# Kernel optimization log

Hardware: AMD Instinct MI355X
Metric: run time of the kernel (lower is better)

The kernel has to match this reference:

```python
import jax, jax.numpy as jnp
import numpy as np

B, N, D, H = 4, 2048, 512, 8
KD = D // H  # per-head key/value dim = 64
NORM = 1.0 / np.sqrt(KD).astype(np.float32)


def setup_inputs() -> dict:
    key = jax.random.key(0)
    kq, km, k1, k2, k3 = jax.random.split(key, 5)
    s = 1.0 / np.sqrt(D)
    return {
        "queries": jax.random.normal(kq, (B, N, D), dtype=jnp.float32),
        "mask": jax.random.randint(km, (B, N, N), 0, 2).astype(jnp.bool_),
        "Wq": jax.random.normal(k1, (D, D), dtype=jnp.float32) * s,
        "Wk": jax.random.normal(k2, (D, D), dtype=jnp.float32) * s,
        "Wc": jax.random.normal(k3, (D, D), dtype=jnp.float32) * s,
    }


def reference(queries, mask, Wq, Wk, Wc):
    # Self-attention path (keys=None, values=None): V uses key_embed (Wk).
    Q = (queries @ Wq.T).reshape(B, N, H, KD)  # [B,N,H,kd]
    K = (queries @ Wk.T).reshape(B, N, H, KD)
    V = K  # original code: V = key_embed(queries) when values is None
    scores = NORM * jnp.einsum("bqhd,bkhd->bhqk", Q, K)  # [B,H,N,N]
    scores = jnp.where(mask[:, None, :, :], -jnp.inf, scores)
    attn = jax.nn.softmax(scores, axis=-1)
    out = jnp.einsum("bhqk,bkhd->bqhd", attn, V).reshape(B, N, H * KD)
    return out @ Wc.T  # [B,N,D]
```

## Files before the change

### kernel.cpp

```cpp
#include <hip/hip_runtime.h>
#include <math.h>

#define B_ 4
#define N_ 2048
#define D_ 512
#define H_ 8
#define KD_ 64
#define NORM2_ 0.18033688011112042f

typedef __attribute__((ext_vector_type(8))) short short8;
typedef __attribute__((ext_vector_type(4))) float f32x4;
#define MFMA16(a, b, c) __builtin_amdgcn_mfma_f32_16x16x32_bf16(a, b, c, 0, 0, 0)
#define EXP2(x) __builtin_amdgcn_exp2f(x)

static __device__ __forceinline__ ushort f2bf(float x) {
  union { float f; uint32_t u; } v; v.f = x;
  const uint32_t r = v.u + 0x7fffu + ((v.u >> 16) & 1u);
  return (ushort)(r >> 16);
}

static __device__ __forceinline__ void async16(ushort* lds, const ushort* g) {
  __builtin_amdgcn_global_load_lds(
      (const __attribute__((address_space(1))) uint32_t*)g,
      (__attribute__((address_space(3))) uint32_t*)lds, 16, 0, 0);
}

__global__ __launch_bounds__(256) void prep(const float* __restrict__ q,
                                            const int* __restrict__ mask,
                                            const float* __restrict__ wq,
                                            const float* __restrict__ wk,
                                            const float* __restrict__ wc,
                                            ushort* __restrict__ Xb,
                                            ushort* __restrict__ Wb,
                                            uint32_t* __restrict__ pk) {
  const int bx = blockIdx.x;
  if (bx < 2048) {
    const int lane = threadIdx.x & 63;
    const int wid = ((bx << 8) + threadIdx.x) >> 6;
    for (int i = wid; i < 65536; i += 8192) {
      const int4 m = ((const int4*)mask)[i * 64 + lane];
      uint32_t nib = (uint32_t)(m.x != 0) | ((uint32_t)(m.y != 0) << 1) |
                     ((uint32_t)(m.z != 0) << 2) | ((uint32_t)(m.w != 0) << 3);
      nib |= __shfl_xor(nib, 1) << 4;
      nib |= __shfl_xor(nib, 2) << 8;
      nib |= __shfl_xor(nib, 4) << 16;
      if ((lane & 7) == 0) pk[i * 8 + (lane >> 3)] = nib;
    }
  } else if (bx < 3072) {
    const int i = ((bx - 2048) << 8) + threadIdx.x;
    for (int j = i; j < 1048576; j += 262144) {
      const float4 v = ((const float4*)q)[j];
      ushort4 o; o.x = f2bf(v.x); o.y = f2bf(v.y); o.z = f2bf(v.z); o.w = f2bf(v.w);
      ((ushort4*)Xb)[j] = o;
    }
  } else {
    const int i = ((bx - 3072) << 8) + threadIdx.x;
    for (int j = i; j < 196608; j += 24576) {
      const int wi = j >> 16, off = j & 65535;
      const float* src = (wi == 0) ? wq : (wi == 1) ? wk : wc;
      const float4 v = ((const float4*)src)[off];
      ushort4 o; o.x = f2bf(v.x); o.y = f2bf(v.y); o.z = f2bf(v.z); o.w = f2bf(v.w);
      ((ushort4*)Wb)[j] = o;
    }
  }
}

template <int F32OUT>
__global__ __launch_bounds__(256) void gemm128(const ushort* __restrict__ X,
                                               const ushort* __restrict__ W0,
                                               const ushort* __restrict__ W1,
                                               void* __restrict__ C0,
                                               void* __restrict__ C1,
                                               float s0, float s1) {
  const ushort* Wp = (blockIdx.z == 0) ? W0 : W1;
  void* Cp = (blockIdx.z == 0) ? C0 : C1;
  const float sc = (blockIdx.z == 0) ? s0 : s1;
  const int t = threadIdx.x;
  const int w = t >> 6, lane = t & 63, quad = lane >> 4, c = lane & 15;
  const int wm = w & 1, wn = w >> 1;
  const int n0 = blockIdx.x * 128, m0 = blockIdx.y * 128;
  __shared__ __align__(16) ushort Xs[128][64];
  __shared__ __align__(16) ushort Ws[128][64];
  f32x4 acc[4][4];
#pragma unroll
  for (int i = 0; i < 4; ++i)
#pragma unroll
    for (int j = 0; j < 4; ++j) acc[i][j] = (f32x4){0.f, 0.f, 0.f, 0.f};

  for (int k0 = 0; k0 < D_; k0 += 64) {
    __syncthreads();
#pragma unroll
    for (int g = 0; g < 4; ++g) {
      const int id = w * 256 + g * 64 + lane;
      const int row = id >> 3, lch = id & 7;
      const int gch = lch ^ (row & 7);
      async16(&Xs[row][lch * 8], X + (size_t)(m0 + row) * D_ + k0 + gch * 8);
      async16(&Ws[row][lch * 8], Wp + (size_t)(n0 + row) * D_ + k0 + gch * 8);
    }
    __syncthreads();
#pragma unroll
    for (int s = 0; s < 2; ++s) {
      short8 af[4], bt[4];
#pragma unroll
      for (int i = 0; i < 4; ++i) {
        const int rA = wn * 64 + i * 16 + c;
        af[i] = *(const short8*)&Ws[rA][(((s * 4 + quad) ^ (rA & 7)) & 7) * 8];
        const int rB = wm * 64 + i * 16 + c;
        bt[i] = *(const short8*)&Xs[rB][(((s * 4 + quad) ^ (rB & 7)) & 7) * 8];
      }
#pragma unroll
      for (int i = 0; i < 4; ++i)
#pragma unroll
        for (int j = 0; j < 4; ++j) acc[i][j] = MFMA16(af[i], bt[j], acc[i][j]);
    }
  }
#pragma unroll
  for (int i = 0; i < 4; ++i)
#pragma unroll
    for (int j = 0; j < 4; ++j) {
      const size_t off =
          (size_t)(m0 + wm * 64 + j * 16 + c) * D_ + n0 + wn * 64 + i * 16 + quad * 4;
      if (F32OUT) {
        float4 v; v.x = acc[i][j][0]; v.y = acc[i][j][1]; v.z = acc[i][j][2]; v.w = acc[i][j][3];
        *(float4*)((float*)Cp + off) = v;
      } else {
        ushort4 v; v.x = f2bf(acc[i][j][0] * sc); v.y = f2bf(acc[i][j][1] * sc);
        v.z = f2bf(acc[i][j][2] * sc); v.w = f2bf(acc[i][j][3] * sc);
        *(ushort4*)((ushort*)Cp + off) = v;
      }
    }
}

__global__ __launch_bounds__(256) void attn_mfma(const ushort* __restrict__ Qb,
                                                 const ushort* __restrict__ Kb,
                                                 const uint32_t* __restrict__ pk,
                                                 ushort* __restrict__ Ab) {
  const int qt = blockIdx.x, h = blockIdx.y, b = blockIdx.z;
  const int q0 = qt * 64;
  const int t = threadIdx.x;
  const int w = t >> 6, lane = t & 63, quad = lane >> 4, c = lane & 15;

  __shared__ __align__(16) ushort Qs[64][64];
  __shared__ __align__(16) ushort Ks[64][64];
  __shared__ __align__(16) uint32_t KtU[64][32];
  __shared__ __align__(16) ushort Pq[4][16][72];

#pragma unroll
  for (int g = 0; g < 2; ++g) {
    const int id = (w << 7) + (g << 6) + lane;
    const int row = id >> 3, lch = id & 7;
    const int gch = lch ^ (row & 7);
    async16(&Qs[row][lch * 8], Qb + (size_t)(b * N_ + q0 + row) * D_ + h * 64 + gch * 8);
  }
  __syncthreads();
  const int rq = (w << 4) + c;
  const short8 bq0 = *(const short8*)&Qs[rq][((quad ^ (rq & 7)) & 7) * 8];
  const short8 bq1 = *(const short8*)&Qs[rq][(((4 + quad) ^ (rq & 7)) & 7) * 8];

  float lacc = 0.f;
  f32x4 o[4];
#pragma unroll
  for (int i = 0; i < 4; ++i) o[i] = (f32x4){0.f, 0.f, 0.f, 0.f};

  const int kp = t >> 3, ch = t & 7;
  const ushort* kb0 = Kb + (size_t)(b * N_ + 2 * kp) * D_ + h * 64 + ch * 8;
  const uint32_t* pkq = pk + ((size_t)(b * N_ + q0 + (w << 4) + c) << 6);

  uint4 c0 = *(const uint4*)kb0;
  uint4 c1 = *(const uint4*)(kb0 + D_);
  uint2 cm = *(const uint2*)pkq;
  uint4 nx0, nx1; uint2 nxm;

  const int NT = N_ / 64;
  for (int kt = 0; kt < NT; ++kt) {
    __syncthreads();
    const int r0 = 2 * kp, r1 = r0 + 1;
    *(uint4*)&Ks[r0][((ch ^ (r0 & 7)) & 7) * 8] = c0;
    *(uint4*)&Ks[r1][((ch ^ (r1 & 7)) & 7) * 8] = c1;
    const uint32_t* a0 = (const uint32_t*)&c0;
    const uint32_t* a1 = (const uint32_t*)&c1;
#pragma unroll
    for (int m = 0; m < 4; ++m) {
      const uint32_t lo = __builtin_amdgcn_perm(a1[m], a0[m], 0x05040100);
      const uint32_t hi = __builtin_amdgcn_perm(a1[m], a0[m], 0x07060302);
      const int j0 = 2 * m, j1 = 2 * m + 1;
      KtU[ch * 8 + j0][(kp & 3) | ((((kp >> 2) ^ j0 ^ ch) & 7) << 2)] = lo;
      KtU[ch * 8 + j1][(kp & 3) | ((((kp >> 2) ^ j1 ^ ch) & 7) << 2)] = hi;
    }
    __syncthreads();

    if (kt + 1 < NT) {
      const ushort* kbn = kb0 + (size_t)(kt + 1) * 64 * D_;
      nx0 = *(const uint4*)kbn;
      nx1 = *(const uint4*)(kbn + D_);
      nxm = *(const uint2*)(pkq + (kt + 1) * 2);
    }

#pragma unroll
    for (int tI = 0; tI < 4; ++tI) {
      const int rk = tI * 16 + c;
      const short8 aK0 = *(const short8*)&Ks[rk][((quad ^ (rk & 7)) & 7) * 8];
      const short8 aK1 = *(const short8*)&Ks[rk][(((4 + quad) ^ (rk & 7)) & 7) * 8];
      f32x4 z = (f32x4){0.f, 0.f, 0.f, 0.f};
      z = MFMA16(aK0, bq0, z);
      z = MFMA16(aK1, bq1, z);
      const uint32_t mw = (tI < 2) ? cm.x : cm.y;
      const int bb = ((tI & 1) << 4) + quad * 4;
      float p[4];
#pragma unroll
      for (int r = 0; r < 4; ++r) {
        const float sv = ((mw >> (bb + r)) & 1u) ? -INFINITY : z[r];
        p[r] = EXP2(sv);
        lacc += p[r];
      }
      const uint32_t pw0 =
          __builtin_amdgcn_perm(__float_as_uint(p[1]), __float_as_uint(p[0]), 0x07060302);
      const uint32_t pw1 =
          __builtin_amdgcn_perm(__float_as_uint(p[3]), __float_as_uint(p[2]), 0x07060302);
      *(uint2*)&Pq[w][c][tI * 16 + quad * 4] = make_uint2(pw0, pw1);
    }

    const short8 bp0 = *(const short8*)&Pq[w][c][quad * 8];
    const short8 bp1 = *(const short8*)&Pq[w][c][32 + quad * 8];
#pragma unroll
    for (int dt = 0; dt < 4; ++dt) {
      const int dd = dt * 16 + c;
      const int g = (c & 7) ^ ((2 * dt + (c >> 3)) & 7);
      const short8 aV0 = *(const short8*)&KtU[dd][((quad ^ g) & 7) << 2];
      const short8 aV1 = *(const short8*)&KtU[dd][(((4 + quad) ^ g) & 7) << 2];
      o[dt] = MFMA16(aV0, bp0, o[dt]);
      o[dt] = MFMA16(aV1, bp1, o[dt]);
    }

    if (kt + 1 < NT) { c0 = nx0; c1 = nx1; cm = nxm; }
  }

  float l = lacc;
  l += __shfl_xor(l, 16);
  l += __shfl_xor(l, 32);
  const float inv = 1.f / l;
#pragma unroll
  for (int dt = 0; dt < 4; ++dt) {
    ushort4 v; v.x = f2bf(o[dt][0] * inv); v.y = f2bf(o[dt][1] * inv);
    v.z = f2bf(o[dt][2] * inv); v.w = f2bf(o[dt][3] * inv);
    *(ushort4*)(Ab + (size_t)(b * N_ + q0 + (w << 4) + c) * D_ + h * 64 + dt * 16 + quad * 4) = v;
  }
}

extern "C" void kernel_launch(void* const* d_in, const int* in_sizes, int n_in,
                              void* d_out, int out_size, void* d_ws, size_t ws_size,
                              hipStream_t stream) {
  const float* queries = (const float*)d_in[0];
  const int* mask = (const int*)d_in[1];
  const float* Wq = (const float*)d_in[2];
  const float* Wk = (const float*)d_in[3];
  const float* Wc = (const float*)d_in[4];
  float* out = (float*)d_out;

  const size_t nTok = (size_t)B_ * N_;
  const size_t nXD = nTok * D_;
  const size_t nW = (size_t)D_ * D_;
  ushort* Xb = (ushort*)d_ws;
  ushort* Wqb = Xb + nXD;
  ushort* Wkb = Wqb + nW;
  ushort* Wcb = Wkb + nW;
  ushort* Qb = Wcb + nW;
  ushort* Kb = Qb + nXD;
  ushort* Ab = Kb + nXD;
  uint32_t* pk = (uint32_t*)(Ab + nXD);

  prep<<<3168, 256, 0, stream>>>(queries, mask, Wq, Wk, Wc, Xb, Wqb, pk);
  gemm128<0><<<dim3(D_ / 128, (int)(nTok / 128), 2), 256, 0, stream>>>(
      Xb, Wqb, Wkb, Qb, Kb, NORM2_, 1.0f);
  attn_mfma<<<dim3(N_ / 64, H_, B_), 256, 0, stream>>>(Qb, Kb, pk, Ab);
  gemm128<1><<<dim3(D_ / 128, (int)(nTok / 128), 1), 256, 0, stream>>>(
      Ab, Wcb, nullptr, out, nullptr, 1.0f, 1.0f);
}
```

Baseline: 214.2 us.

## Fuse all stages into one cooperative persistent kernel with grid syncs

Replaces the four separate launches (prep, QK projection GEMM, attention, output GEMM) with a single cooperative kernel of 1024 blocks that runs each stage in turn, separated by grid-wide syncs. The GEMMs move to 64x64 tiles done in place, and the attention row sum is now computed with an MFMA against a ones vector instead of a scalar accumulation. The aim is to remove launch gaps and inter-kernel drain. In exchange it adds grid.sync costs, smaller GEMM tiles, and occupancy limits from cooperative launch, with a fallback to the old path if the launch fails.

Result: slower. 556.3 us (+159.7%).

```diff
diff --git a/kernel.cpp b/kernel.cpp
--- a/kernel.cpp
+++ b/kernel.cpp
@@ -1,11 +1,13 @@
 #include <hip/hip_runtime.h>
+#include <hip/hip_cooperative_groups.h>
 #include <math.h>
+
+namespace cg = cooperative_groups;
 
 #define B_ 4
 #define N_ 2048
 #define D_ 512
 #define H_ 8
-#define KD_ 64
 #define NORM2_ 0.18033688011112042f
 
 typedef __attribute__((ext_vector_type(8))) short short8;
@@ -23,6 +25,236 @@
   __builtin_amdgcn_global_load_lds(
       (const __attribute__((address_space(1))) uint32_t*)g,
       (__attribute__((address_space(3))) uint32_t*)lds, 16, 0, 0);
+}
+
+template <int NZ, int F32OUT>
+static __device__ __forceinline__ void gemm64(const ushort* __restrict__ X,
+                                              const ushort* __restrict__ Wa,
+                                              const ushort* __restrict__ Wb,
+                                              void* __restrict__ Ca,
+                                              void* __restrict__ Cb, float sA,
+                                              int tt, int nf, char* smem, int t) {
+  ushort(*Xs)[64] = (ushort(*)[64])smem;
+  ushort(*WsA)[64] = (ushort(*)[64])(smem + 8192);
+  ushort(*WsB)[64] = (ushort(*)[64])(smem + 16384);
+  const int w = t >> 6, lane = t & 63, quad = lane >> 4, c = lane & 15;
+  const int m0 = tt * 64, n0 = nf * 64;
+  f32x4 acc[NZ][4];
+#pragma unroll
+  for (int z = 0; z < NZ; ++z)
+#pragma unroll
+    for (int i = 0; i < 4; ++i) acc[z][i] = (f32x4){0.f, 0.f, 0.f, 0.f};
+
+  for (int k0 = 0; k0 < D_; k0 += 64) {
+    __syncthreads();
+#pragma unroll
+    for (int p = 0; p < 2; ++p) {
+      const int id = t + p * 256;
+      const int row = id >> 3, lch = id & 7, gch = lch ^ (row & 7);
+      async16(&Xs[row][lch * 8], X + (size_t)(m0 + row) * D_ + k0 + gch * 8);
+      async16(&WsA[row][lch * 8], Wa + (size_t)(n0 + row) * D_ + k0 + gch * 8);
+      if (NZ == 2)
+        async16(&WsB[row][lch * 8], Wb + (size_t)(n0 + row) * D_ + k0 + gch * 8);
+    }
+    __syncthreads();
+#pragma unroll
+    for (int s = 0; s < 2; ++s) {
+      const int rB = w * 16 + c;
+      const short8 bt = *(const short8*)&Xs[rB][(((s * 4 + quad) ^ (rB & 7)) & 7) * 8];
+#pragma unroll
+      for (int i = 0; i < 4; ++i) {
+        const int rA = i * 16 + c;
+        const int col = (((s * 4 + quad) ^ (rA & 7)) & 7) * 8;
+        acc[0][i] = MFMA16(*(const short8*)&WsA[rA][col], bt, acc[0][i]);
+        if (NZ == 2) acc[1][i] = MFMA16(*(const short8*)&WsB[rA][col], bt, acc[1][i]);
+      }
+    }
+  }
+  const int token = m0 + w * 16 + c;
+#pragma unroll
+  for (int i = 0; i < 4; ++i) {
+    const size_t off = (size_t)token * D_ + n0 + i * 16 + quad * 4;
+    if (F32OUT) {
+      float4 v;
+      v.x = acc[0][i][0]; v.y = acc[0][i][1]; v.z = acc[0][i][2]; v.w = acc[0][i][3];
+      *(float4*)((float*)Ca + off) = v;
+    } else {
+      ushort4 va;
+      va.x = f2bf(acc[0][i][0] * sA); va.y = f2bf(acc[0][i][1] * sA);
+      va.z = f2bf(acc[0][i][2] * sA); va.w = f2bf(acc[0][i][3] * sA);
+      *(ushort4*)((ushort*)Ca + off) = va;
+      if (NZ == 2) {
+        ushort4 vb;
+        vb.x = f2bf(acc[1][i][0]); vb.y = f2bf(acc[1][i][1]);
+        vb.z = f2bf(acc[1][i][2]); vb.w = f2bf(acc[1][i][3]);
+        *(ushort4*)((ushort*)Cb + off) = vb;
+      }
+    }
+  }
+}
+
+template <int JPB, int MW>
+__global__ __launch_bounds__(256, MW) void fused_mha(
+    const float* __restrict__ queries, const int* __restrict__ mask,
+    const float* __restrict__ Wq, const float* __restrict__ Wk,
+    const float* __restrict__ Wc, float* __restrict__ out,
+    ushort* __restrict__ Xb, ushort* __restrict__ Wqb, ushort* __restrict__ Wkb,
+    ushort* __restrict__ Wcb, ushort* __restrict__ Qb, ushort* __restrict__ Kb,
+    ushort* __restrict__ Ab, uint32_t* __restrict__ pk) {
+  __shared__ __align__(16) char smem[33792];
+  const int t = threadIdx.x;
+  const int bx = blockIdx.x;
+  const int nblk = 1024 / JPB;
+  cg::grid_group grid = cg::this_grid();
+
+  {
+    const int nth = nblk << 8, nwv = nblk << 2;
+    const int tid = (bx << 8) + t;
+    const int lane = t & 63;
+    const int wid = tid >> 6;
+    for (int i = wid; i < 65536; i += nwv) {
+      const int4 m = ((const int4*)mask)[(size_t)i * 64 + lane];
+      uint32_t nib = (uint32_t)(m.x != 0) | ((uint32_t)(m.y != 0) << 1) |
+                     ((uint32_t)(m.z != 0) << 2) | ((uint32_t)(m.w != 0) << 3);
+      nib |= __shfl_xor(nib, 1) << 4;
+      nib |= __shfl_xor(nib, 2) << 8;
+      nib |= __shfl_xor(nib, 4) << 16;
+      if ((lane & 7) == 0) pk[i * 8 + (lane >> 3)] = nib;
+    }
+    for (int j = tid; j < 1048576; j += nth) {
+      const float4 v = ((const float4*)queries)[j];
+      ushort4 o; o.x = f2bf(v.x); o.y = f2bf(v.y); o.z = f2bf(v.z); o.w = f2bf(v.w);
+      ((ushort4*)Xb)[j] = o;
+    }
+    for (int j = tid; j < 196608; j += nth) {
+      const int wi = j >> 16, off = j & 65535;
+      const float* src = (wi == 0) ? Wq : (wi == 1) ? Wk : Wc;
+      const float4 v = ((const float4*)src)[off];
+      ushort4 o; o.x = f2bf(v.x); o.y = f2bf(v.y); o.z = f2bf(v.z); o.w = f2bf(v.w);
+      ((ushort4*)Wqb)[j] = o;
+    }
+  }
+  grid.sync();
+
+  for (int job = bx; job < 1024; job += nblk)
+    gemm64<2, 0>(Xb, Wqb, Wkb, Qb, Kb, NORM2_, job >> 3, job & 7, smem, t);
+  grid.sync();
+
+  for (int job = bx; job < 1024; job += nblk) {
+    const int b = job >> 8, h = (job >> 5) & 7, qt = job & 31;
+    const int q0 = qt * 64;
+    const int w = t >> 6, lane = t & 63, quad = lane >> 4, c = lane & 15;
+    ushort(*Qs)[64] = (ushort(*)[64])smem;
+    ushort(*Ks)[64] = (ushort(*)[64])(smem + 8192);
+    uint32_t(*KtU)[32] = (uint32_t(*)[32])(smem + 16384);
+    ushort(*Pq)[16][72] = (ushort(*)[16][72])(smem + 24576);
+
+    __syncthreads();
+#pragma unroll
+    for (int p = 0; p < 2; ++p) {
+      const int id = t + p * 256;
+      const int row = id >> 3, lch = id & 7, gch = lch ^ (row & 7);
+      async16(&Qs[row][lch * 8], Qb + (size_t)(b * N_ + q0 + row) * D_ + h * 64 + gch * 8);
+    }
+    __syncthreads();
+    const int rq = (w << 4) + c;
+    const short8 bq0 = *(const short8*)&Qs[rq][((quad ^ (rq & 7)) & 7) * 8];
+    const short8 bq1 = *(const short8*)&Qs[rq][(((4 + quad) ^ (rq & 7)) & 7) * 8];
+
+    short8 vones;
+#pragma unroll
+    for (int i = 0; i < 8; ++i) vones[i] = (short)0x3F80;
+
+    f32x4 o[4];
+#pragma unroll
+    for (int i = 0; i < 4; ++i) o[i] = (f32x4){0.f, 0.f, 0.f, 0.f};
+    f32x4 o5 = (f32x4){0.f, 0.f, 0.f, 0.f};
+
+    const int kp = t >> 3, ch = t & 7;
+    const ushort* kb0 = Kb + (size_t)(b * N_ + 2 * kp) * D_ + h * 64 + ch * 8;
+    const uint32_t* pkq = pk + ((size_t)(b * N_ + q0 + (w << 4) + c) << 6);
+
+    uint4 c0 = *(const uint4*)kb0;
+    uint4 c1 = *(const uint4*)(kb0 + D_);
+    uint2 cm = *(const uint2*)pkq;
+    uint4 nx0, nx1; uint2 nxm;
+
+    const int NT = N_ / 64;
+    for (int kt = 0; kt < NT; ++kt) {
+      __syncthreads();
+      const int r0 = 2 * kp, r1 = r0 + 1;
+      *(uint4*)&Ks[r0][((ch ^ (r0 & 7)) & 7) * 8] = c0;
+      *(uint4*)&Ks[r1][((ch ^ (r1 & 7)) & 7) * 8] = c1;
+      const uint32_t* a0 = (const uint32_t*)&c0;
+      const uint32_t* a1 = (const uint32_t*)&c1;
+#pragma unroll
+      for (int m = 0; m < 4; ++m) {
+        const uint32_t lo = __builtin_amdgcn_perm(a1[m], a0[m], 0x05040100);
+        const uint32_t hi = __builtin_amdgcn_perm(a1[m], a0[m], 0x07060302);
+        const int j0 = 2 * m, j1 = 2 * m + 1;
+        KtU[ch * 8 + j0][(kp & 3) | ((((kp >> 2) ^ j0 ^ ch) & 7) << 2)] = lo;
+        KtU[ch * 8 + j1][(kp & 3) | ((((kp >> 2) ^ j1 ^ ch) & 7) << 2)] = hi;
+      }
+      __syncthreads();
+
+      if (kt + 1 < NT) {
+        const ushort* kbn = kb0 + (size_t)(kt + 1) * 64 * D_;
+        nx0 = *(const uint4*)kbn;
+        nx1 = *(const uint4*)(kbn + D_);
+        nxm = *(const uint2*)(pkq + (kt + 1) * 2);
+      }
+
+#pragma unroll
+      for (int tI = 0; tI < 4; ++tI) {
+        const int rk = tI * 16 + c;
+        const short8 aK0 = *(const short8*)&Ks[rk][((quad ^ (rk & 7)) & 7) * 8];
+        const short8 aK1 = *(const short8*)&Ks[rk][(((4 + quad) ^ (rk & 7)) & 7) * 8];
+        f32x4 z = (f32x4){0.f, 0.f, 0.f, 0.f};
+        z = MFMA16(aK0, bq0, z);
+        z = MFMA16(aK1, bq1, z);
+        const uint32_t mw = (tI < 2) ? cm.x : cm.y;
+        const int bb = ((tI & 1) << 4) + quad * 4;
+        uint32_t pb[4];
+#pragma unroll
+        for (int r = 0; r < 4; ++r) {
+          const float sv = ((mw >> (bb + r)) & 1u) ? -INFINITY : z[r];
+          pb[r] = __float_as_uint(EXP2(sv));
+        }
+        const uint32_t pw0 = __builtin_amdgcn_perm(pb[1], pb[0], 0x07060302);
+        const uint32_t pw1 = __builtin_amdgcn_perm(pb[3], pb[2], 0x07060302);
+        *(uint2*)&Pq[w][c][tI * 16 + quad * 4] = make_uint2(pw0, pw1);
+      }
+
+      const short8 bp0 = *(const short8*)&Pq[w][c][quad * 8];
+      const short8 bp1 = *(const short8*)&Pq[w][c][32 + quad * 8];
+      o5 = MFMA16(vones, bp0, o5);
+      o5 = MFMA16(vones, bp1, o5);
+#pragma unroll
+      for (int dt = 0; dt < 4; ++dt) {
+        const int dd = dt * 16 + c;
+        const int g = (c & 7) ^ ((2 * dt + (c >> 3)) & 7);
+        const short8 aV0 = *(const short8*)&KtU[dd][((quad ^ g) & 7) << 2];
+        const short8 aV1 = *(const short8*)&KtU[dd][(((4 + quad) ^ g) & 7) << 2];
+        o[dt] = MFMA16(aV0, bp0, o[dt]);
+        o[dt] = MFMA16(aV1, bp1, o[dt]);
+      }
+
+      if (kt + 1 < NT) { c0 = nx0; c1 = nx1; cm = nxm; }
+    }
+
+    const float inv = 1.f / o5[0];
+#pragma unroll
+    for (int dt = 0; dt < 4; ++dt) {
+      ushort4 v; v.x = f2bf(o[dt][0] * inv); v.y = f2bf(o[dt][1] * inv);
+      v.z = f2bf(o[dt][2] * inv); v.w = f2bf(o[dt][3] * inv);
+      *(ushort4*)(Ab + (size_t)(b * N_ + q0 + (w << 4) + c) * D_ + h * 64 +
+                  dt * 16 + quad * 4) = v;
+    }
+  }
+  grid.sync();
+
+  for (int job = bx; job < 1024; job += nblk)
+    gemm64<1, 1>(Ab, Wcb, nullptr, out, nullptr, 1.0f, job >> 3, job & 7, smem, t);
 }
 
 __global__ __launch_bounds__(256) void prep(const float* __restrict__ q,
@@ -38,7 +270,7 @@
     const int lane = threadIdx.x & 63;
     const int wid = ((bx << 8) + threadIdx.x) >> 6;
     for (int i = wid; i < 65536; i += 8192) {
-      const int4 m = ((const int4*)mask)[i * 64 + lane];
+      const int4 m = ((const int4*)mask)[(size_t)i * 64 + lane];
       uint32_t nib = (uint32_t)(m.x != 0) | ((uint32_t)(m.y != 0) << 1) |
                      ((uint32_t)(m.z != 0) << 2) | ((uint32_t)(m.w != 0) << 3);
       nib |= __shfl_xor(nib, 1) << 4;
@@ -146,10 +378,9 @@
   __shared__ __align__(16) ushort Pq[4][16][72];
 
 #pragma unroll
-  for (int g = 0; g < 2; ++g) {
-    const int id = (w << 7) + (g << 6) + lane;
-    const int row = id >> 3, lch = id & 7;
-    const int gch = lch ^ (row & 7);
+  for (int p = 0; p < 2; ++p) {
+    const int id = t + p * 256;
+    const int row = id >> 3, lch = id & 7, gch = lch ^ (row & 7);
     async16(&Qs[row][lch * 8], Qb + (size_t)(b * N_ + q0 + row) * D_ + h * 64 + gch * 8);
   }
   __syncthreads();
@@ -269,10 +500,25 @@
   ushort* Ab = Kb + nXD;
   uint32_t* pk = (uint32_t*)(Ab + nXD);
 
-  prep<<<3168, 256, 0, stream>>>(queries, mask, Wq, Wk, Wc, Xb, Wqb, pk);
-  gemm128<0><<<dim3(D_ / 128, (int)(nTok / 128), 2), 256, 0, stream>>>(
-      Xb, Wqb, Wkb, Qb, Kb, NORM2_, 1.0f);
-  attn_mfma<<<dim3(N_ / 64, H_, B_), 256, 0, stream>>>(Qb, Kb, pk, Ab);
-  gemm128<1><<<dim3(D_ / 128, (int)(nTok / 128), 1), 256, 0, stream>>>(
-      Ab, Wcb, nullptr, out, nullptr, 1.0f, 1.0f);
-}
+  void* args[] = {(void*)&queries, (void*)&mask, (void*)&Wq, (void*)&Wk,
+                  (void*)&Wc,      (void*)&out,  (void*)&Xb, (void*)&Wqb,
+                  (void*)&Wkb,     (void*)&Wcb,  (void*)&Qb, (void*)&Kb,
+                  (void*)&Ab,      (void*)&pk};
+
+  hipError_t e = hipLaunchCooperativeKernel(
+      reinterpret_cast<void*>(&fused_mha<1, 4>), dim3(1024), dim3(256), args, 0, stream);
+  if (e != hipSuccess) {
+    (void)hipGetLastError();
+    e = hipLaunchCooperativeKernel(
+        reinterpret_cast<void*>(&fused_mha<2, 2>), dim3(512), dim3(256), args, 0, stream);
+  }
+  if (e != hipSuccess) {
+    (void)hipGetLastError();
+    prep<<<3168, 256, 0, stream>>>(queries, mask, Wq, Wk, Wc, Xb, Wqb, pk);
+    gemm128<0><<<dim3(D_ / 128, (int)(nTok / 128), 2), 256, 0, stream>>>(
+        Xb, Wqb, Wkb, Qb, Kb, NORM2_, 1.0f);
+    attn_mfma<<<dim3(N_ / 64, H_, B_), 256, 0, stream>>>(Qb, Kb, pk, Ab);
+    gemm128<1><<<dim3(D_ / 128, (int)(nTok / 128), 1), 256, 0, stream>>>(
+        Ab, Wcb, nullptr, out, nullptr, 1.0f, 1.0f);
+  }
+}
```

## Fuse fp32-to-bf16 conversion into GEMMs and merge mask packing into QK GEMM launch

Applied to the files above, without the earlier changes.

Removes the separate prep kernel. The QK projection GEMM now reads fp32 inputs and weights directly and converts them to bf16 while staging into LDS, and the mask-packing work runs in extra blocks of the same launch. The output GEMM converts Wc on the fly, and attention aliases the Q staging buffer with the P buffer to reduce LDS use. This cuts one launch and the bf16 copy round trip through global memory. In exchange, the GEMMs lose async global-to-LDS loads for the converted operands, re-read fp32 data per tile, and repeat the conversion work in every tile.

After: 226.0 us. +5.5%, slower.

```diff
diff --git a/kernel.cpp b/kernel.cpp
--- a/kernel.cpp
+++ b/kernel.cpp
@@ -1,11 +1,11 @@
 #include <hip/hip_runtime.h>
+#include <hip/hip_bf16.h>
 #include <math.h>
 
 #define B_ 4
 #define N_ 2048
 #define D_ 512
 #define H_ 8
-#define KD_ 64
 #define NORM2_ 0.18033688011112042f
 
 typedef __attribute__((ext_vector_type(8))) short short8;
@@ -13,32 +13,34 @@
 #define MFMA16(a, b, c) __builtin_amdgcn_mfma_f32_16x16x32_bf16(a, b, c, 0, 0, 0)
 #define EXP2(x) __builtin_amdgcn_exp2f(x)
 
-static __device__ __forceinline__ ushort f2bf(float x) {
-  union { float f; uint32_t u; } v; v.f = x;
-  const uint32_t r = v.u + 0x7fffu + ((v.u >> 16) & 1u);
-  return (ushort)(r >> 16);
-}
-
-static __device__ __forceinline__ void async16(ushort* lds, const ushort* g) {
+static __device__ __forceinline__ uint32_t pk2(float lo, float hi) {
+  __hip_bfloat162 h = __float22bfloat162_rn(make_float2(lo, hi));
+  return *(reinterpret_cast<uint32_t*>(&h));
+}
+
+static __device__ __forceinline__ void async16(const ushort* lds, const ushort* g) {
   __builtin_amdgcn_global_load_lds(
       (const __attribute__((address_space(1))) uint32_t*)g,
-      (__attribute__((address_space(3))) uint32_t*)lds, 16, 0, 0);
-}
-
-__global__ __launch_bounds__(256) void prep(const float* __restrict__ q,
-                                            const int* __restrict__ mask,
-                                            const float* __restrict__ wq,
-                                            const float* __restrict__ wk,
-                                            const float* __restrict__ wc,
-                                            ushort* __restrict__ Xb,
-                                            ushort* __restrict__ Wb,
-                                            uint32_t* __restrict__ pk) {
+      (__attribute__((address_space(3))) uint32_t*)(ushort*)lds, 16, 0, 0);
+}
+
+__global__ __launch_bounds__(256) void gemmqk_pack(const float* __restrict__ X,
+                                                   const float* __restrict__ Wq,
+                                                   const float* __restrict__ Wk,
+                                                   const int* __restrict__ mask,
+                                                   ushort* __restrict__ Qb,
+                                                   ushort* __restrict__ Kb,
+                                                   uint32_t* __restrict__ pk) {
+  __shared__ __align__(16) ushort Xs[128][64];
+  __shared__ __align__(16) ushort Ws[128][64];
   const int bx = blockIdx.x;
-  if (bx < 2048) {
-    const int lane = threadIdx.x & 63;
-    const int wid = ((bx << 8) + threadIdx.x) >> 6;
-    for (int i = wid; i < 65536; i += 8192) {
-      const int4 m = ((const int4*)mask)[i * 64 + lane];
+  const int t = threadIdx.x;
+
+  if (bx >= 512) {
+    const int lane = t & 63;
+    const int wid = (((bx - 512) << 8) + t) >> 6;
+    for (int i = wid; i < 65536; i += 2048) {
+      const int4 m = ((const int4*)mask)[(size_t)i * 64 + lane];
       uint32_t nib = (uint32_t)(m.x != 0) | ((uint32_t)(m.y != 0) << 1) |
                      ((uint32_t)(m.z != 0) << 2) | ((uint32_t)(m.w != 0) << 3);
       nib |= __shfl_xor(nib, 1) << 4;
@@ -46,41 +48,17 @@
       nib |= __shfl_xor(nib, 4) << 16;
       if ((lane & 7) == 0) pk[i * 8 + (lane >> 3)] = nib;
     }
-  } else if (bx < 3072) {
-    const int i = ((bx - 2048) << 8) + threadIdx.x;
-    for (int j = i; j < 1048576; j += 262144) {
-      const float4 v = ((const float4*)q)[j];
-      ushort4 o; o.x = f2bf(v.x); o.y = f2bf(v.y); o.z = f2bf(v.z); o.w = f2bf(v.w);
-      ((ushort4*)Xb)[j] = o;
-    }
-  } else {
-    const int i = ((bx - 3072) << 8) + threadIdx.x;
-    for (int j = i; j < 196608; j += 24576) {
-      const int wi = j >> 16, off = j & 65535;
-      const float* src = (wi == 0) ? wq : (wi == 1) ? wk : wc;
-      const float4 v = ((const float4*)src)[off];
-      ushort4 o; o.x = f2bf(v.x); o.y = f2bf(v.y); o.z = f2bf(v.z); o.w = f2bf(v.w);
-      ((ushort4*)Wb)[j] = o;
-    }
-  }
-}
-
-template <int F32OUT>
-__global__ __launch_bounds__(256) void gemm128(const ushort* __restrict__ X,
-                                               const ushort* __restrict__ W0,
-                                               const ushort* __restrict__ W1,
-                                               void* __restrict__ C0,
-                                               void* __restrict__ C1,
-                                               float s0, float s1) {
-  const ushort* Wp = (blockIdx.z == 0) ? W0 : W1;
-  void* Cp = (blockIdx.z == 0) ? C0 : C1;
-  const float sc = (blockIdx.z == 0) ? s0 : s1;
-  const int t = threadIdx.x;
+    return;
+  }
+
+  const float* Wp = (bx >> 8) ? Wk : Wq;
+  ushort* Cp = (bx >> 8) ? Kb : Qb;
+  const float sc = (bx >> 8) ? 1.0f : NORM2_;
+  const int tile = bx & 255;
+  const int n0 = (tile & 3) * 128, m0 = (tile >> 2) * 128;
   const int w = t >> 6, lane = t & 63, quad = lane >> 4, c = lane & 15;
   const int wm = w & 1, wn = w >> 1;
-  const int n0 = blockIdx.x * 128, m0 = blockIdx.y * 128;
-  __shared__ __align__(16) ushort Xs[128][64];
-  __shared__ __align__(16) ushort Ws[128][64];
+
   f32x4 acc[4][4];
 #pragma unroll
   for (int i = 0; i < 4; ++i)
@@ -92,10 +70,21 @@
 #pragma unroll
     for (int g = 0; g < 4; ++g) {
       const int id = w * 256 + g * 64 + lane;
-      const int row = id >> 3, lch = id & 7;
-      const int gch = lch ^ (row & 7);
-      async16(&Xs[row][lch * 8], X + (size_t)(m0 + row) * D_ + k0 + gch * 8);
-      async16(&Ws[row][lch * 8], Wp + (size_t)(n0 + row) * D_ + k0 + gch * 8);
+      const int row = id >> 3, lch = id & 7, gch = lch ^ (row & 7);
+      const float* xs = X + (size_t)(m0 + row) * D_ + k0 + gch * 8;
+      const float4 xa = *(const float4*)xs;
+      const float4 xb = *(const float4*)(xs + 4);
+      uint4 u;
+      u.x = pk2(xa.x, xa.y); u.y = pk2(xa.z, xa.w);
+      u.z = pk2(xb.x, xb.y); u.w = pk2(xb.z, xb.w);
+      *(uint4*)&Xs[row][lch * 8] = u;
+      const float* ws = Wp + (size_t)(n0 + row) * D_ + k0 + gch * 8;
+      const float4 wa = *(const float4*)ws;
+      const float4 wb = *(const float4*)(ws + 4);
+      uint4 v;
+      v.x = pk2(wa.x, wa.y); v.y = pk2(wa.z, wa.w);
+      v.z = pk2(wb.x, wb.y); v.w = pk2(wb.z, wb.w);
+      *(uint4*)&Ws[row][lch * 8] = v;
     }
     __syncthreads();
 #pragma unroll
@@ -120,14 +109,10 @@
     for (int j = 0; j < 4; ++j) {
       const size_t off =
           (size_t)(m0 + wm * 64 + j * 16 + c) * D_ + n0 + wn * 64 + i * 16 + quad * 4;
-      if (F32OUT) {
-        float4 v; v.x = acc[i][j][0]; v.y = acc[i][j][1]; v.z = acc[i][j][2]; v.w = acc[i][j][3];
-        *(float4*)((float*)Cp + off) = v;
-      } else {
-        ushort4 v; v.x = f2bf(acc[i][j][0] * sc); v.y = f2bf(acc[i][j][1] * sc);
-        v.z = f2bf(acc[i][j][2] * sc); v.w = f2bf(acc[i][j][3] * sc);
-        *(ushort4*)((ushort*)Cp + off) = v;
-      }
+      uint2 uv;
+      uv.x = pk2(acc[i][j][0] * sc, acc[i][j][1] * sc);
+      uv.y = pk2(acc[i][j][2] * sc, acc[i][j][3] * sc);
+      *(uint2*)(Cp + off) = uv;
     }
 }
 
@@ -140,16 +125,16 @@
   const int t = threadIdx.x;
   const int w = t >> 6, lane = t & 63, quad = lane >> 4, c = lane & 15;
 
-  __shared__ __align__(16) ushort Qs[64][64];
   __shared__ __align__(16) ushort Ks[64][64];
   __shared__ __align__(16) uint32_t KtU[64][32];
-  __shared__ __align__(16) ushort Pq[4][16][72];
-
-#pragma unroll
-  for (int g = 0; g < 2; ++g) {
-    const int id = (w << 7) + (g << 6) + lane;
-    const int row = id >> 3, lch = id & 7;
-    const int gch = lch ^ (row & 7);
+  __shared__ __align__(16) ushort QP[4][16][72];
+  ushort(*Qs)[64] = (ushort(*)[64]) & QP[0][0][0];
+  ushort(*Pq)[16][72] = QP;
+
+#pragma unroll
+  for (int p = 0; p < 2; ++p) {
+    const int id = t + p * 256;
+    const int row = id >> 3, lch = id & 7, gch = lch ^ (row & 7);
     async16(&Qs[row][lch * 8], Qb + (size_t)(b * N_ + q0 + row) * D_ + h * 64 + gch * 8);
   }
   __syncthreads();
@@ -241,10 +226,70 @@
   const float inv = 1.f / l;
 #pragma unroll
   for (int dt = 0; dt < 4; ++dt) {
-    ushort4 v; v.x = f2bf(o[dt][0] * inv); v.y = f2bf(o[dt][1] * inv);
-    v.z = f2bf(o[dt][2] * inv); v.w = f2bf(o[dt][3] * inv);
-    *(ushort4*)(Ab + (size_t)(b * N_ + q0 + (w << 4) + c) * D_ + h * 64 + dt * 16 + quad * 4) = v;
-  }
+    uint2 uv;
+    uv.x = pk2(o[dt][0] * inv, o[dt][1] * inv);
+    uv.y = pk2(o[dt][2] * inv, o[dt][3] * inv);
+    *(uint2*)(Ab + (size_t)(b * N_ + q0 + (w << 4) + c) * D_ + h * 64 + dt * 16 + quad * 4) = uv;
+  }
+}
+
+__global__ __launch_bounds__(256) void gemmout(const ushort* __restrict__ A,
+                                               const float* __restrict__ Wc,
+                                               float* __restrict__ out) {
+  __shared__ __align__(16) ushort Xs[128][64];
+  __shared__ __align__(16) ushort Ws[128][64];
+  const int t = threadIdx.x;
+  const int w = t >> 6, lane = t & 63, quad = lane >> 4, c = lane & 15;
+  const int wm = w & 1, wn = w >> 1;
+  const int n0 = blockIdx.x * 128, m0 = blockIdx.y * 128;
+  f32x4 acc[4][4];
+#pragma unroll
+  for (int i = 0; i < 4; ++i)
+#pragma unroll
+    for (int j = 0; j < 4; ++j) acc[i][j] = (f32x4){0.f, 0.f, 0.f, 0.f};
+
+  for (int k0 = 0; k0 < D_; k0 += 64) {
+    __syncthreads();
+#pragma unroll
+    for (int g = 0; g < 4; ++g) {
+      const int id = w * 256 + g * 64 + lane;
+      const int row = id >> 3, lch = id & 7, gch = lch ^ (row & 7);
+      async16(&Xs[row][lch * 8], A + (size_t)(m0 + row) * D_ + k0 + gch * 8);
+      const float* ws = Wc + (size_t)(n0 + row) * D_ + k0 + gch * 8;
+      const float4 wa = *(const float4*)ws;
+      const float4 wb = *(const float4*)(ws + 4);
+      uint4 v;
+      v.x = pk2(wa.x, wa.y); v.y = pk2(wa.z, wa.w);
+      v.z = pk2(wb.x, wb.y); v.w = pk2(wb.z, wb.w);
+      *(uint4*)&Ws[row][lch * 8] = v;
+    }
+    __syncthreads();
+#pragma unroll
+    for (int s = 0; s < 2; ++s) {
+      short8 af[4], bt[4];
+#pragma unroll
+      for (int i = 0; i < 4; ++i) {
+        const int rA = wn * 64 + i * 16 + c;
+        af[i] = *(const short8*)&Ws[rA][(((s * 4 + quad) ^ (rA & 7)) & 7) * 8];
+        const int rB = wm * 64 + i * 16 + c;
+        bt[i] = *(const short8*)&Xs[rB][(((s * 4 + quad) ^ (rB & 7)) & 7) * 8];
+      }
+#pragma unroll
+      for (int i = 0; i < 4; ++i)
+#pragma unroll
+        for (int j = 0; j < 4; ++j) acc[i][j] = MFMA16(af[i], bt[j], acc[i][j]);
+    }
+  }
+#pragma unroll
+  for (int i = 0; i < 4; ++i)
+#pragma unroll
+    for (int j = 0; j < 4; ++j) {
+      const size_t off =
+          (size_t)(m0 + wm * 64 + j * 16 + c) * D_ + n0 + wn * 64 + i * 16 + quad * 4;
+      float4 v;
+      v.x = acc[i][j][0]; v.y = acc[i][j][1]; v.z = acc[i][j][2]; v.w = acc[i][j][3];
+      *(float4*)(out + off) = v;
+    }
 }
 
 extern "C" void kernel_launch(void* const* d_in, const int* in_sizes, int n_in,
@@ -257,22 +302,13 @@
   const float* Wc = (const float*)d_in[4];
   float* out = (float*)d_out;
 
-  const size_t nTok = (size_t)B_ * N_;
-  const size_t nXD = nTok * D_;
-  const size_t nW = (size_t)D_ * D_;
-  ushort* Xb = (ushort*)d_ws;
-  ushort* Wqb = Xb + nXD;
-  ushort* Wkb = Wqb + nW;
-  ushort* Wcb = Wkb + nW;
-  ushort* Qb = Wcb + nW;
+  const size_t nXD = (size_t)B_ * N_ * D_;
+  ushort* Qb = (ushort*)d_ws;
   ushort* Kb = Qb + nXD;
   ushort* Ab = Kb + nXD;
   uint32_t* pk = (uint32_t*)(Ab + nXD);
 
-  prep<<<3168, 256, 0, stream>>>(queries, mask, Wq, Wk, Wc, Xb, Wqb, pk);
-  gemm128<0><<<dim3(D_ / 128, (int)(nTok / 128), 2), 256, 0, stream>>>(
-      Xb, Wqb, Wkb, Qb, Kb, NORM2_, 1.0f);
+  gemmqk_pack<<<1024, 256, 0, stream>>>(queries, Wq, Wk, mask, Qb, Kb, pk);
   attn_mfma<<<dim3(N_ / 64, H_, B_), 256, 0, stream>>>(Qb, Kb, pk, Ab);
-  gemm128<1><<<dim3(D_ / 128, (int)(nTok / 128), 1), 256, 0, stream>>>(
-      Ab, Wcb, nullptr, out, nullptr, 1.0f, 1.0f);
-}
+  gemmout<<<dim3(D_ / 128, (B_ * N_) / 128), 256, 0, stream>>>(Ab, Wc, out);
+}
```

## Double-buffer K tiles in attention, compute row sums via MFMA, use bf16 pack intrinsic

Applied to the files above, without the earlier changes.

The attention kernel now double-buffers the K and transposed-K LDS tiles, writing the next tile after the current tile's MFMAs so only one barrier per iteration remains. The softmax denominator is computed by an extra MFMA against a ones vector rather than per-lane float adds and shuffles, so it sums the bf16-rounded probabilities. Q staging shares LDS with the P buffer, and bf16 conversions use the packed HIP intrinsic. The changes raise LDS use per block and add an MFMA per tile, which may reduce occupancy.

Measured after the change: 218.9 us. +2.2%, slower.

```diff
diff --git a/kernel.cpp b/kernel.cpp
--- a/kernel.cpp
+++ b/kernel.cpp
@@ -1,11 +1,11 @@
 #include <hip/hip_runtime.h>
+#include <hip/hip_bf16.h>
 #include <math.h>
 
 #define B_ 4
 #define N_ 2048
 #define D_ 512
 #define H_ 8
-#define KD_ 64
 #define NORM2_ 0.18033688011112042f
 
 typedef __attribute__((ext_vector_type(8))) short short8;
@@ -19,10 +19,15 @@
   return (ushort)(r >> 16);
 }
 
-static __device__ __forceinline__ void async16(ushort* lds, const ushort* g) {
+static __device__ __forceinline__ uint32_t pk2(float lo, float hi) {
+  __hip_bfloat162 h = __float22bfloat162_rn(make_float2(lo, hi));
+  return *(reinterpret_cast<uint32_t*>(&h));
+}
+
+static __device__ __forceinline__ void async16(const ushort* lds, const ushort* g) {
   __builtin_amdgcn_global_load_lds(
       (const __attribute__((address_space(1))) uint32_t*)g,
-      (__attribute__((address_space(3))) uint32_t*)lds, 16, 0, 0);
+      (__attribute__((address_space(3))) uint32_t*)(ushort*)lds, 16, 0, 0);
 }
 
 __global__ __launch_bounds__(256) void prep(const float* __restrict__ q,
@@ -38,7 +43,7 @@
     const int lane = threadIdx.x & 63;
     const int wid = ((bx << 8) + threadIdx.x) >> 6;
     for (int i = wid; i < 65536; i += 8192) {
-      const int4 m = ((const int4*)mask)[i * 64 + lane];
+      const int4 m = ((const int4*)mask)[(size_t)i * 64 + lane];
       uint32_t nib = (uint32_t)(m.x != 0) | ((uint32_t)(m.y != 0) << 1) |
                      ((uint32_t)(m.z != 0) << 2) | ((uint32_t)(m.w != 0) << 3);
       nib |= __shfl_xor(nib, 1) << 4;
@@ -50,8 +55,8 @@
     const int i = ((bx - 2048) << 8) + threadIdx.x;
     for (int j = i; j < 1048576; j += 262144) {
       const float4 v = ((const float4*)q)[j];
-      ushort4 o; o.x = f2bf(v.x); o.y = f2bf(v.y); o.z = f2bf(v.z); o.w = f2bf(v.w);
-      ((ushort4*)Xb)[j] = o;
+      uint2 o; o.x = pk2(v.x, v.y); o.y = pk2(v.z, v.w);
+      ((uint2*)Xb)[j] = o;
     }
   } else {
     const int i = ((bx - 3072) << 8) + threadIdx.x;
@@ -59,8 +64,8 @@
       const int wi = j >> 16, off = j & 65535;
       const float* src = (wi == 0) ? wq : (wi == 1) ? wk : wc;
       const float4 v = ((const float4*)src)[off];
-      ushort4 o; o.x = f2bf(v.x); o.y = f2bf(v.y); o.z = f2bf(v.z); o.w = f2bf(v.w);
-      ((ushort4*)Wb)[j] = o;
+      uint2 o; o.x = pk2(v.x, v.y); o.y = pk2(v.z, v.w);
+      ((uint2*)Wb)[j] = o;
     }
   }
 }
@@ -124,9 +129,10 @@
         float4 v; v.x = acc[i][j][0]; v.y = acc[i][j][1]; v.z = acc[i][j][2]; v.w = acc[i][j][3];
         *(float4*)((float*)Cp + off) = v;
       } else {
-        ushort4 v; v.x = f2bf(acc[i][j][0] * sc); v.y = f2bf(acc[i][j][1] * sc);
-        v.z = f2bf(acc[i][j][2] * sc); v.w = f2bf(acc[i][j][3] * sc);
-        *(ushort4*)((ushort*)Cp + off) = v;
+        uint2 uv;
+        uv.x = pk2(acc[i][j][0] * sc, acc[i][j][1] * sc);
+        uv.y = pk2(acc[i][j][2] * sc, acc[i][j][3] * sc);
+        *(uint2*)((ushort*)Cp + off) = uv;
       }
     }
 }
@@ -140,16 +146,16 @@
   const int t = threadIdx.x;
   const int w = t >> 6, lane = t & 63, quad = lane >> 4, c = lane & 15;
 
-  __shared__ __align__(16) ushort Qs[64][64];
-  __shared__ __align__(16) ushort Ks[64][64];
-  __shared__ __align__(16) uint32_t KtU[64][32];
-  __shared__ __align__(16) ushort Pq[4][16][72];
-
-#pragma unroll
-  for (int g = 0; g < 2; ++g) {
-    const int id = (w << 7) + (g << 6) + lane;
-    const int row = id >> 3, lch = id & 7;
-    const int gch = lch ^ (row & 7);
+  __shared__ __align__(16) ushort Ks[2][64][64];
+  __shared__ __align__(16) uint32_t KtU[2][64][32];
+  __shared__ __align__(16) ushort QP[4][16][72];
+  ushort(*Qs)[64] = (ushort(*)[64]) & QP[0][0][0];
+  ushort(*Pq)[16][72] = QP;
+
+#pragma unroll
+  for (int p = 0; p < 2; ++p) {
+    const int id = t + p * 256;
+    const int row = id >> 3, lch = id & 7, gch = lch ^ (row & 7);
     async16(&Qs[row][lch * 8], Qb + (size_t)(b * N_ + q0 + row) * D_ + h * 64 + gch * 8);
   }
   __syncthreads();
@@ -157,26 +163,26 @@
   const short8 bq0 = *(const short8*)&Qs[rq][((quad ^ (rq & 7)) & 7) * 8];
   const short8 bq1 = *(const short8*)&Qs[rq][(((4 + quad) ^ (rq & 7)) & 7) * 8];
 
-  float lacc = 0.f;
+  short8 vones;
+#pragma unroll
+  for (int i = 0; i < 8; ++i) vones[i] = (short)0x3F80;
+
   f32x4 o[4];
 #pragma unroll
   for (int i = 0; i < 4; ++i) o[i] = (f32x4){0.f, 0.f, 0.f, 0.f};
+  f32x4 o5 = (f32x4){0.f, 0.f, 0.f, 0.f};
 
   const int kp = t >> 3, ch = t & 7;
+  const int r0 = 2 * kp, r1 = r0 + 1;
+  const int ksw0 = ((ch ^ (r0 & 7)) & 7) * 8, ksw1 = ((ch ^ (r1 & 7)) & 7) * 8;
   const ushort* kb0 = Kb + (size_t)(b * N_ + 2 * kp) * D_ + h * 64 + ch * 8;
   const uint32_t* pkq = pk + ((size_t)(b * N_ + q0 + (w << 4) + c) << 6);
 
-  uint4 c0 = *(const uint4*)kb0;
-  uint4 c1 = *(const uint4*)(kb0 + D_);
-  uint2 cm = *(const uint2*)pkq;
-  uint4 nx0, nx1; uint2 nxm;
-
-  const int NT = N_ / 64;
-  for (int kt = 0; kt < NT; ++kt) {
-    __syncthreads();
-    const int r0 = 2 * kp, r1 = r0 + 1;
-    *(uint4*)&Ks[r0][((ch ^ (r0 & 7)) & 7) * 8] = c0;
-    *(uint4*)&Ks[r1][((ch ^ (r1 & 7)) & 7) * 8] = c1;
+  {
+    const uint4 c0 = *(const uint4*)kb0;
+    const uint4 c1 = *(const uint4*)(kb0 + D_);
+    *(uint4*)&Ks[0][r0][ksw0] = c0;
+    *(uint4*)&Ks[0][r1][ksw1] = c1;
     const uint32_t* a0 = (const uint32_t*)&c0;
     const uint32_t* a1 = (const uint32_t*)&c1;
 #pragma unroll
@@ -184,12 +190,20 @@
       const uint32_t lo = __builtin_amdgcn_perm(a1[m], a0[m], 0x05040100);
       const uint32_t hi = __builtin_amdgcn_perm(a1[m], a0[m], 0x07060302);
       const int j0 = 2 * m, j1 = 2 * m + 1;
-      KtU[ch * 8 + j0][(kp & 3) | ((((kp >> 2) ^ j0 ^ ch) & 7) << 2)] = lo;
-      KtU[ch * 8 + j1][(kp & 3) | ((((kp >> 2) ^ j1 ^ ch) & 7) << 2)] = hi;
-    }
+      KtU[0][ch * 8 + j0][(kp & 3) | ((((kp >> 2) ^ j0 ^ ch) & 7) << 2)] = lo;
+      KtU[0][ch * 8 + j1][(kp & 3) | ((((kp >> 2) ^ j1 ^ ch) & 7) << 2)] = hi;
+    }
+  }
+  uint2 cm = *(const uint2*)pkq;
+
+  const int NT = N_ / 64;
+  for (int kt = 0; kt < NT; ++kt) {
     __syncthreads();
-
-    if (kt + 1 < NT) {
+    const int cur = kt & 1, nxt = cur ^ 1;
+
+    uint4 nx0, nx1; uint2 nxm;
+    const bool more = (kt + 1 < NT);
+    if (more) {
       const ushort* kbn = kb0 + (size_t)(kt + 1) * 64 * D_;
       nx0 = *(const uint4*)kbn;
       nx1 = *(const uint4*)(kbn + D_);
@@ -199,51 +213,62 @@
 #pragma unroll
     for (int tI = 0; tI < 4; ++tI) {
       const int rk = tI * 16 + c;
-      const short8 aK0 = *(const short8*)&Ks[rk][((quad ^ (rk & 7)) & 7) * 8];
-      const short8 aK1 = *(const short8*)&Ks[rk][(((4 + quad) ^ (rk & 7)) & 7) * 8];
+      const short8 aK0 = *(const short8*)&Ks[cur][rk][((quad ^ (rk & 7)) & 7) * 8];
+      const short8 aK1 = *(const short8*)&Ks[cur][rk][(((4 + quad) ^ (rk & 7)) & 7) * 8];
       f32x4 z = (f32x4){0.f, 0.f, 0.f, 0.f};
       z = MFMA16(aK0, bq0, z);
       z = MFMA16(aK1, bq1, z);
       const uint32_t mw = (tI < 2) ? cm.x : cm.y;
       const int bb = ((tI & 1) << 4) + quad * 4;
-      float p[4];
+      uint32_t pb[4];
 #pragma unroll
       for (int r = 0; r < 4; ++r) {
         const float sv = ((mw >> (bb + r)) & 1u) ? -INFINITY : z[r];
-        p[r] = EXP2(sv);
-        lacc += p[r];
+        pb[r] = __float_as_uint(EXP2(sv));
       }
-      const uint32_t pw0 =
-          __builtin_amdgcn_perm(__float_as_uint(p[1]), __float_as_uint(p[0]), 0x07060302);
-      const uint32_t pw1 =
-          __builtin_amdgcn_perm(__float_as_uint(p[3]), __float_as_uint(p[2]), 0x07060302);
+      const uint32_t pw0 = __builtin_amdgcn_perm(pb[1], pb[0], 0x07060302);
+      const uint32_t pw1 = __builtin_amdgcn_perm(pb[3], pb[2], 0x07060302);
       *(uint2*)&Pq[w][c][tI * 16 + quad * 4] = make_uint2(pw0, pw1);
     }
 
     const short8 bp0 = *(const short8*)&Pq[w][c][quad * 8];
     const short8 bp1 = *(const short8*)&Pq[w][c][32 + quad * 8];
+    o5 = MFMA16(vones, bp0, o5);
+    o5 = MFMA16(vones, bp1, o5);
 #pragma unroll
     for (int dt = 0; dt < 4; ++dt) {
       const int dd = dt * 16 + c;
       const int g = (c & 7) ^ ((2 * dt + (c >> 3)) & 7);
-      const short8 aV0 = *(const short8*)&KtU[dd][((quad ^ g) & 7) << 2];
-      const short8 aV1 = *(const short8*)&KtU[dd][(((4 + quad) ^ g) & 7) << 2];
+      const short8 aV0 = *(const short8*)&KtU[cur][dd][((quad ^ g) & 7) << 2];
+      const short8 aV1 = *(const short8*)&KtU[cur][dd][(((4 + quad) ^ g) & 7) << 2];
       o[dt] = MFMA16(aV0, bp0, o[dt]);
       o[dt] = MFMA16(aV1, bp1, o[dt]);
     }
 
-    if (kt + 1 < NT) { c0 = nx0; c1 = nx1; cm = nxm; }
-  }
-
-  float l = lacc;
-  l += __shfl_xor(l, 16);
-  l += __shfl_xor(l, 32);
-  const float inv = 1.f / l;
+    if (more) {
+      *(uint4*)&Ks[nxt][r0][ksw0] = nx0;
+      *(uint4*)&Ks[nxt][r1][ksw1] = nx1;
+      const uint32_t* a0 = (const uint32_t*)&nx0;
+      const uint32_t* a1 = (const uint32_t*)&nx1;
+#pragma unroll
+      for (int m = 0; m < 4; ++m) {
+        const uint32_t lo = __builtin_amdgcn_perm(a1[m], a0[m], 0x05040100);
+        const uint32_t hi = __builtin_amdgcn_perm(a1[m], a0[m], 0x07060302);
+        const int j0 = 2 * m, j1 = 2 * m + 1;
+        KtU[nxt][ch * 8 + j0][(kp & 3) | ((((kp >> 2) ^ j0 ^ ch) & 7) << 2)] = lo;
+        KtU[nxt][ch * 8 + j1][(kp & 3) | ((((kp >> 2) ^ j1 ^ ch) & 7) << 2)] = hi;
+      }
+      cm = nxm;
+    }
+  }
+
+  const float inv = 1.f / o5[0];
 #pragma unroll
   for (int dt = 0; dt < 4; ++dt) {
-    ushort4 v; v.x = f2bf(o[dt][0] * inv); v.y = f2bf(o[dt][1] * inv);
-    v.z = f2bf(o[dt][2] * inv); v.w = f2bf(o[dt][3] * inv);
-    *(ushort4*)(Ab + (size_t)(b * N_ + q0 + (w << 4) + c) * D_ + h * 64 + dt * 16 + quad * 4) = v;
+    uint2 uv;
+    uv.x = pk2(o[dt][0] * inv, o[dt][1] * inv);
+    uv.y = pk2(o[dt][2] * inv, o[dt][3] * inv);
+    *(uint2*)(Ab + (size_t)(b * N_ + q0 + (w << 4) + c) * D_ + h * 64 + dt * 16 + quad * 4) = uv;
   }
 }
 
```
